# Optimization experiments

Measured on AMD Instinct MI355X. Metric: run time of the kernel, lower is better.

Reference implementation:

```python
import jax, jax.numpy as jnp
import numpy as np

C = 256
NUM_HEADS = 4
GROUPS = 32  # max(1, 256//8), divides 256
EPS = 1e-5


def setup_inputs() -> dict:
    key = jax.random.key(0)
    ks = jax.random.split(key, 7)
    B, H, W = 4, 64, 64
    s = 0.02
    return {
        "x": jax.random.normal(ks[0], (B, C, H, W), dtype=jnp.float32),
        "norm_gamma": jnp.ones((C,), jnp.float32),
        "norm_beta": jnp.zeros((C,), jnp.float32),
        "qkv_w": jax.random.normal(ks[1], (3 * C, C), jnp.float32) * s,  # 1x1 conv kernel squeezed
        "qkv_b": jax.random.normal(ks[2], (3 * C,), jnp.float32) * s,
        "proj_w": jax.random.normal(ks[3], (C, C), jnp.float32) * s,
        "proj_b": jax.random.normal(ks[4], (C,), jnp.float32) * s,
    }


def reference(x, norm_gamma, norm_beta, qkv_w, qkv_b, proj_w, proj_b):
    B, Cc, H, W = x.shape
    hd = Cc // NUM_HEADS
    scale = hd ** -0.5

    # GroupNorm over (channels-per-group, H, W)
    xg = x.reshape(B, GROUPS, Cc // GROUPS, H, W)
    mu = xg.mean(axis=(2, 3, 4), keepdims=True)
    var = xg.var(axis=(2, 3, 4), keepdims=True)
    h = ((xg - mu) * jax.lax.rsqrt(var + EPS)).reshape(B, Cc, H, W)
    h = h * norm_gamma[:, None, None] + norm_beta[:, None, None]

    # 1x1 conv QKV: [B,3C,H,W]
    qkv = jnp.einsum('bchw,oc->bohw', h, qkv_w) + qkv_b[:, None, None]
    q, k, v = jnp.split(qkv, 3, axis=1)

    def heads(t):  # [B,C,H,W] -> [B,nh,HW,hd]
        return t.reshape(B, NUM_HEADS, hd, H * W).transpose(0, 1, 3, 2)

    q, k, v = heads(q), heads(k), heads(v)
    attn = jnp.einsum('bhnd,bhmd->bhnm', q, k) * scale  # [B,nh,HW,HW]
    attn = jax.nn.softmax(attn, axis=-1)
    out = jnp.einsum('bhnm,bhmd->bhnd', attn, v)  # [B,nh,HW,hd]
    out = out.transpose(0, 1, 3, 2).reshape(B, Cc, H, W)

    out = jnp.einsum('bchw,oc->bohw', out, proj_w) + proj_b[:, None, None]
    return x + out
```

## Files before the change

### kernel.cpp

```cpp
#include <hip/hip_runtime.h>
#include <hip/hip_bf16.h>
#include <stdint.h>

typedef unsigned short u16;
typedef __attribute__((ext_vector_type(8))) short bf16x8;
typedef __attribute__((ext_vector_type(4))) float f32x4;
typedef __attribute__((ext_vector_type(16))) float f32x16;

#define HW 4096
#define CC 256
#define QSCALE 0.18033688011112042f

__device__ __forceinline__ u16 f2bf(float f) {
    union { float f; uint32_t i; } v; v.f = f;
    uint32_t x = v.i;
    return (u16)((x + 0x7fffu + ((x >> 16) & 1u)) >> 16);
}

__device__ __forceinline__ float fast_exp2(float x) {
#if __has_builtin(__builtin_amdgcn_exp2f)
    return __builtin_amdgcn_exp2f(x);
#else
    return exp2f(x);
#endif
}

__device__ __forceinline__ unsigned cvt_pk_bf16(float lo, float hi) {
    unsigned r;
    asm("v_cvt_pk_bf16_f32 %0, %1, %2" : "=v"(r) : "v"(lo), "v"(hi));
    return r;
}

__device__ __forceinline__ void plane_swap(unsigned& a, unsigned& b) {
#if __has_builtin(__builtin_amdgcn_permlane32_swap)
    auto r = __builtin_amdgcn_permlane32_swap(a, b, false, false);
    a = r[0]; b = r[1];
#else
    unsigned ax = __shfl_xor((int)a, 32);
    unsigned bx = __shfl_xor((int)b, 32);
    bool hi = (threadIdx.x & 32) != 0;
    unsigned na = hi ? bx : a;
    unsigned nb = hi ? b : ax;
    a = na; b = nb;
#endif
}

#define MFMA16(a, b, c) __builtin_amdgcn_mfma_f32_16x16x32_bf16(a, b, c, 0, 0, 0)
#define MFMA32(a, b, c) __builtin_amdgcn_mfma_f32_32x32x16_bf16(a, b, c, 0, 0, 0)

__global__ void k_wsc(const float* __restrict__ qkv_w, const float* __restrict__ proj_w,
                      const float* __restrict__ x,
                      u16* __restrict__ wqkv, u16* __restrict__ wproj, float* __restrict__ stats) {
    int bid = blockIdx.x;
    if (bid < 128) {
        int bg = bid;
        const float4* p = reinterpret_cast<const float4*>(x + (size_t)bg * 8 * HW);
        float s = 0.f, ss = 0.f;
        for (int i = 0; i < 32; ++i) {
            float4 v = p[threadIdx.x + i * 256];
            s += v.x + v.y + v.z + v.w;
            ss += v.x * v.x + v.y * v.y + v.z * v.z + v.w * v.w;
        }
        __shared__ float rs[256], rss[256];
        rs[threadIdx.x] = s; rss[threadIdx.x] = ss;
        __syncthreads();
        for (int off = 128; off > 0; off >>= 1) {
            if (threadIdx.x < off) { rs[threadIdx.x] += rs[threadIdx.x + off]; rss[threadIdx.x] += rss[threadIdx.x + off]; }
            __syncthreads();
        }
        if (threadIdx.x == 0) {
            float mu = rs[0] * (1.f / 32768.f);
            float var = rss[0] * (1.f / 32768.f) - mu * mu;
            stats[bg * 2] = mu;
            stats[bg * 2 + 1] = rsqrtf(var + 1e-5f);
        }
    } else {
        int i = (bid - 128) * 256 + threadIdx.x;
        if (i < 768 * 256) {
            int o = i >> 8;
            float sc = (o < 256) ? QSCALE : 1.0f;
            wqkv[i] = f2bf(qkv_w[i] * sc);
        }
        int j = i - 768 * 256;
        if (j >= 0 && j < 256 * 256) wproj[j] = f2bf(proj_w[j]);
    }
}

__global__ __launch_bounds__(256) void k_gnt(const float* __restrict__ x, const float* __restrict__ stats,
                                             const float* __restrict__ gamma, const float* __restrict__ beta,
                                             u16* __restrict__ h_t) {
    int bid = blockIdx.x;
    int b = bid >> 8;
    int cb = (bid >> 6) & 3;
    int nb = bid & 63;
    int t = threadIdx.x;
    int cl = t >> 2;
    int ch = t & 3;
    int c = cb * 64 + cl;
    int g = c >> 3;
    float mu = stats[(b * 32 + g) * 2];
    float rsg = stats[(b * 32 + g) * 2 + 1];
    float ga = gamma[c], be = beta[c];
    __shared__ float T[64][66];
    const float4* p = reinterpret_cast<const float4*>(x + ((size_t)(b * CC + c)) * HW + nb * 64 + ch * 16);
    for (int j = 0; j < 4; ++j) {
        float4 v = p[j];
        int nbase = ch * 16 + j * 4;
        T[nbase + 0][cl] = (v.x - mu) * rsg * ga + be;
        T[nbase + 1][cl] = (v.y - mu) * rsg * ga + be;
        T[nbase + 2][cl] = (v.z - mu) * rsg * ga + be;
        T[nbase + 3][cl] = (v.w - mu) * rsg * ga + be;
    }
    __syncthreads();
    int nl = t >> 2;
    union { u16 u[16]; uint4 q[2]; } pk;
    for (int j = 0; j < 16; ++j) pk.u[j] = f2bf(T[nl][ch * 16 + j]);
    u16* dst = h_t + ((size_t)b * HW + nb * 64 + nl) * CC + cb * 64 + ch * 16;
    *reinterpret_cast<uint4*>(dst) = pk.q[0];
    *reinterpret_cast<uint4*>(dst + 8) = pk.q[1];
}

__global__ __launch_bounds__(256) void k_qkv(const u16* __restrict__ wqkv, const u16* __restrict__ h_t,
                                             const float* __restrict__ qkv_b,
                                             u16* __restrict__ qk_t, u16* __restrict__ v_o) {
    int bid = blockIdx.x;
    int b = bid / 192;
    int rem = bid % 192;
    int om = rem >> 5;
    int nb = rem & 31;
    int o0 = om * 128, n0 = nb * 128;
    int t = threadIdx.x;
    int wid = t >> 6, lane = t & 63;
    int wm = wid >> 1, wn = wid & 1;
    int l15 = lane & 15, lg = lane >> 4;

    __shared__ u16 sA[128 * 40], sB[128 * 40];
    f32x4 acc[4][4];
    for (int i = 0; i < 4; ++i) for (int j = 0; j < 4; ++j) acc[i][j] = (f32x4)0.f;

    const u16* gA = wqkv + (size_t)o0 * 256;
    const u16* gB = h_t + ((size_t)b * HW + n0) * CC;
    int row = t >> 1, half = t & 1;

    for (int kt = 0; kt < 8; ++kt) {
        __syncthreads();
        {
            const uint4* pa = reinterpret_cast<const uint4*>(gA + (size_t)row * 256 + kt * 32 + half * 16);
            uint4 a0 = pa[0], a1 = pa[1];
            const uint4* pb = reinterpret_cast<const uint4*>(gB + (size_t)row * 256 + kt * 32 + half * 16);
            uint4 b0 = pb[0], b1 = pb[1];
            *reinterpret_cast<uint4*>(&sA[row * 40 + half * 16]) = a0;
            *reinterpret_cast<uint4*>(&sA[row * 40 + half * 16 + 8]) = a1;
            *reinterpret_cast<uint4*>(&sB[row * 40 + half * 16]) = b0;
            *reinterpret_cast<uint4*>(&sB[row * 40 + half * 16 + 8]) = b1;
        }
        __syncthreads();
        bf16x8 af[4], bfr[4];
        for (int mt = 0; mt < 4; ++mt)
            af[mt] = *reinterpret_cast<const bf16x8*>(&sA[(wm * 64 + mt * 16 + l15) * 40 + lg * 8]);
        for (int nt = 0; nt < 4; ++nt)
            bfr[nt] = *reinterpret_cast<const bf16x8*>(&sB[(wn * 64 + nt * 16 + l15) * 40 + lg * 8]);
        for (int mt = 0; mt < 4; ++mt)
            for (int nt = 0; nt < 4; ++nt)
                acc[mt][nt] = MFMA16(af[mt], bfr[nt], acc[mt][nt]);
    }

    if (o0 < 512) {
        for (int mt = 0; mt < 4; ++mt) {
            int ob = o0 + wm * 64 + mt * 16 + lg * 4;
            float bias[4];
            for (int r = 0; r < 4; ++r) {
                int o = ob + r;
                bias[r] = qkv_b[o] * (o < 256 ? QSCALE : 1.0f);
            }
            for (int nt = 0; nt < 4; ++nt) {
                int n = n0 + wn * 64 + nt * 16 + l15;
                union { u16 u[4]; uint2 q; } pk;
                for (int r = 0; r < 4; ++r) pk.u[r] = f2bf(acc[mt][nt][r] + bias[r]);
                *reinterpret_cast<uint2*>(qk_t + ((size_t)b * HW + n) * 512 + ob) = pk.q;
            }
        }
    } else {
        for (int mt = 0; mt < 4; ++mt) {
            int ob = o0 + wm * 64 + mt * 16 + lg * 4;
            for (int nt = 0; nt < 4; ++nt) {
                int n = n0 + wn * 64 + nt * 16 + l15;
                for (int r = 0; r < 4; ++r) {
                    int o = ob + r;
                    float bias = qkv_b[o];
                    v_o[((size_t)b * 256 + (o - 512)) * HW + n] = f2bf(acc[mt][nt][r] + bias);
                }
            }
        }
    }
}

__global__ __launch_bounds__(256, 4) void k_attn(const u16* __restrict__ qk_t, const u16* __restrict__ v_o,
                                                 u16* __restrict__ ao_t) {
    int bid = blockIdx.x;
    int swz = (bid & 7) * 64 + (bid >> 3);
    int qb = swz & 31, head = (swz >> 5) & 3, b = swz >> 7;
    int n0 = qb * 128;
    int t = threadIdx.x;
    int wq = t >> 6;
    int lane = t & 63, l31 = lane & 31, h = lane >> 5;

    __shared__ u16 lds[2 * 2 * 64 * 72];

    const u16* qbase = qk_t + ((size_t)b * HW + n0 + wq * 32 + l31) * 512 + head * 64 + h * 8;
    bf16x8 qf[4];
#pragma unroll
    for (int cs = 0; cs < 4; ++cs) qf[cs] = *reinterpret_cast<const bf16x8*>(qbase + cs * 16);

    const u16* gK = qk_t + (size_t)b * HW * 512 + 256 + head * 64;
    const u16* gV = v_o + ((size_t)b * 256 + head * 64) * (size_t)HW;

    int sop = t >> 7;
    int tIn = t & 127;
    int srow = tIn >> 1, shalf = tIn & 1;
    const u16* pS;
    long step;
    if (sop == 0) { pS = gK + (size_t)srow * 512 + shalf * 32; step = 64 * 512; }
    else          { pS = gV + (size_t)srow * HW + shalf * 32;  step = 64; }
    uint4 a0 = *reinterpret_cast<const uint4*>(pS);
    uint4 a1 = *reinterpret_cast<const uint4*>(pS + 8);
    uint4 a2 = *reinterpret_cast<const uint4*>(pS + 16);
    uint4 a3 = *reinterpret_cast<const uint4*>(pS + 24);

    f32x16 o0 = (f32x16)0.f, o1 = (f32x16)0.f;
    float l_run = 0.f;

    for (int ti = 0; ti < 64; ++ti) {
        int buf = ti & 1;
        u16* w = lds + buf * 9216 + sop * 4608 + srow * 72 + shalf * 32;
        *reinterpret_cast<uint4*>(w) = a0;
        *reinterpret_cast<uint4*>(w + 8) = a1;
        *reinterpret_cast<uint4*>(w + 16) = a2;
        *reinterpret_cast<uint4*>(w + 24) = a3;
        if (ti < 63) {
            pS += step;
            a0 = *reinterpret_cast<const uint4*>(pS);
            a1 = *reinterpret_cast<const uint4*>(pS + 8);
            a2 = *reinterpret_cast<const uint4*>(pS + 16);
            a3 = *reinterpret_cast<const uint4*>(pS + 24);
        }
        __syncthreads();

        const u16* bK = lds + buf * 9216;
        const u16* bV = bK + 4608;

        f32x16 s0 = (f32x16)0.f, s1 = (f32x16)0.f;
#pragma unroll
        for (int cs = 0; cs < 4; ++cs) {
            bf16x8 k0 = *reinterpret_cast<const bf16x8*>(bK + l31 * 72 + cs * 16 + h * 8);
            bf16x8 k1 = *reinterpret_cast<const bf16x8*>(bK + (l31 + 32) * 72 + cs * 16 + h * 8);
            s0 = MFMA32(k0, qf[cs], s0);
            s1 = MFMA32(k1, qf[cs], s1);
        }

        float ps = 0.f;
#pragma unroll
        for (int i = 0; i < 16; ++i) { float e = fast_exp2(s0[i]); s0[i] = e; ps += e; }
#pragma unroll
        for (int i = 0; i < 16; ++i) { float e = fast_exp2(s1[i]); s1[i] = e; ps += e; }
        l_run += ps;

        unsigned dws[2][8];
#pragma unroll
        for (int a = 0; a < 4; ++a) {
            dws[0][2 * a]     = cvt_pk_bf16(s0[4 * a],     s0[4 * a + 1]);
            dws[0][2 * a + 1] = cvt_pk_bf16(s0[4 * a + 2], s0[4 * a + 3]);
            dws[1][2 * a]     = cvt_pk_bf16(s1[4 * a],     s1[4 * a + 1]);
            dws[1][2 * a + 1] = cvt_pk_bf16(s1[4 * a + 2], s1[4 * a + 3]);
        }
        bf16x8 pf[4];
#pragma unroll
        for (int ks = 0; ks < 4; ++ks) {
            int kt = ks >> 1, sf = ks & 1;
            unsigned A0 = dws[kt][4 * sf + 0], B0 = dws[kt][4 * sf + 2];
            unsigned A1 = dws[kt][4 * sf + 1], B1 = dws[kt][4 * sf + 3];
            plane_swap(A0, B0);
            plane_swap(A1, B1);
            union { unsigned d[4]; bf16x8 v; } u;
            u.d[0] = A0; u.d[1] = A1; u.d[2] = B0; u.d[3] = B1;
            pf[ks] = u.v;
        }

#pragma unroll
        for (int ks = 0; ks < 4; ++ks) {
            bf16x8 v0 = *reinterpret_cast<const bf16x8*>(bV + l31 * 72 + ks * 16 + h * 8);
            bf16x8 v1 = *reinterpret_cast<const bf16x8*>(bV + (l31 + 32) * 72 + ks * 16 + h * 8);
            o0 = MFMA32(v0, pf[ks], o0);
            o1 = MFMA32(v1, pf[ks], o1);
        }
    }

    l_run += __shfl_xor(l_run, 32);
    float inv = 1.0f / l_run;

    u16* E = lds;
    int qrow = wq * 32 + l31;
#pragma unroll
    for (int r = 0; r < 16; ++r) {
        int d = (r & 3) + 8 * (r >> 2) + 4 * h;
        E[qrow * 72 + d]      = f2bf(o0[r] * inv);
        E[qrow * 72 + 32 + d] = f2bf(o1[r] * inv);
    }
    __syncthreads();
#pragma unroll
    for (int i = 0; i < 4; ++i) {
        int item = i * 256 + t;
        int row = item >> 3, cb = item & 7;
        uint4 w = *reinterpret_cast<const uint4*>(E + row * 72 + cb * 8);
        *reinterpret_cast<uint4*>(ao_t + ((size_t)b * HW + n0 + row) * 256 + head * 64 + cb * 8) = w;
    }
}

__global__ __launch_bounds__(256) void k_proj(const u16* __restrict__ wproj, const u16* __restrict__ ao_t,
                                              const float* __restrict__ proj_b, const float* __restrict__ x,
                                              float* __restrict__ out) {
    int bid = blockIdx.x;
    int b = bid >> 6;
    int om = (bid >> 5) & 1;
    int nb = bid & 31;
    int o0 = om * 128, n0 = nb * 128;
    int t = threadIdx.x;
    int wid = t >> 6, lane = t & 63;
    int wm = wid >> 1, wn = wid & 1;
    int l15 = lane & 15, lg = lane >> 4;

    __shared__ u16 sA[128 * 40], sB[128 * 40];
    f32x4 acc[4][4];
    for (int i = 0; i < 4; ++i) for (int j = 0; j < 4; ++j) acc[i][j] = (f32x4)0.f;

    const u16* gA = wproj + (size_t)o0 * 256;
    const u16* gB = ao_t + ((size_t)b * HW + n0) * CC;
    int row = t >> 1, half = t & 1;

    for (int kt = 0; kt < 8; ++kt) {
        __syncthreads();
        {
            const uint4* pa = reinterpret_cast<const uint4*>(gA + (size_t)row * 256 + kt * 32 + half * 16);
            uint4 a0 = pa[0], a1 = pa[1];
            const uint4* pb = reinterpret_cast<const uint4*>(gB + (size_t)row * 256 + kt * 32 + half * 16);
            uint4 b0 = pb[0], b1 = pb[1];
            *reinterpret_cast<uint4*>(&sA[row * 40 + half * 16]) = a0;
            *reinterpret_cast<uint4*>(&sA[row * 40 + half * 16 + 8]) = a1;
            *reinterpret_cast<uint4*>(&sB[row * 40 + half * 16]) = b0;
            *reinterpret_cast<uint4*>(&sB[row * 40 + half * 16 + 8]) = b1;
        }
        __syncthreads();
        bf16x8 af[4], bfr[4];
        for (int mt = 0; mt < 4; ++mt)
            af[mt] = *reinterpret_cast<const bf16x8*>(&sA[(wm * 64 + mt * 16 + l15) * 40 + lg * 8]);
        for (int nt = 0; nt < 4; ++nt)
            bfr[nt] = *reinterpret_cast<const bf16x8*>(&sB[(wn * 64 + nt * 16 + l15) * 40 + lg * 8]);
        for (int mt = 0; mt < 4; ++mt)
            for (int nt = 0; nt < 4; ++nt)
                acc[mt][nt] = MFMA16(af[mt], bfr[nt], acc[mt][nt]);
    }

    for (int mt = 0; mt < 4; ++mt) {
        int ob = o0 + wm * 64 + mt * 16 + lg * 4;
        for (int nt = 0; nt < 4; ++nt) {
            int n = n0 + wn * 64 + nt * 16 + l15;
            for (int r = 0; r < 4; ++r) {
                int o = ob + r;
                size_t idx = ((size_t)(b * CC + o)) * HW + n;
                out[idx] = acc[mt][nt][r] + proj_b[o] + x[idx];
            }
        }
    }
}

extern "C" void kernel_launch(void* const* d_in, const int* in_sizes, int n_in,
                              void* d_out, int out_size, void* d_ws, size_t ws_size,
                              hipStream_t stream) {
    const float* x      = (const float*)d_in[0];
    const float* gamma  = (const float*)d_in[1];
    const float* beta   = (const float*)d_in[2];
    const float* qkv_w  = (const float*)d_in[3];
    const float* qkv_b  = (const float*)d_in[4];
    const float* proj_w = (const float*)d_in[5];
    const float* proj_b = (const float*)d_in[6];
    float* out = (float*)d_out;
    char* ws = (char*)d_ws;

    float* stats = (float*)ws;
    u16* wqkv  = (u16*)(ws + 4096);
    u16* wproj = (u16*)(ws + 4096 + 393216);
    u16* h_t   = (u16*)(ws + 1048576);
    u16* qk_t  = (u16*)(ws + 1048576 + 8388608);
    u16* v_o   = (u16*)(ws + 1048576 + 8388608 + 16777216);
    u16* ao_t  = (u16*)(ws + 1048576 + 8388608 + 16777216 + 8388608);

    k_wsc<<<dim3(1152), dim3(256), 0, stream>>>(qkv_w, proj_w, x, wqkv, wproj, stats);
    k_gnt<<<dim3(1024), dim3(256), 0, stream>>>(x, stats, gamma, beta, h_t);
    k_qkv<<<dim3(768), dim3(256), 0, stream>>>(wqkv, h_t, qkv_b, qk_t, v_o);
    k_attn<<<dim3(512), dim3(256), 0, stream>>>(qk_t, v_o, ao_t);
    k_proj<<<dim3(256), dim3(256), 0, stream>>>(wproj, ao_t, proj_b, x, out);
}
```

Before: 132.4 us.

## Split attention key range across two blocks and add a combine kernel

The attention kernel now splits each query tile's 4096 keys into two halves handled by separate blocks, doubling the grid from 512 to 1024 blocks so more of the GPU is occupied. Each block writes unnormalized fp32 partial outputs and row sums to workspace. A new k_comb kernel adds the two halves, normalizes, and writes the bf16 attention output. The cost is an extra kernel launch and roughly 33 MB of fp32 partial traffic written and read back. The combine relies on the existing softmax using no per-split running max, so the partial sums can be added directly.

```diff
diff --git a/kernel.cpp b/kernel.cpp
--- a/kernel.cpp
+++ b/kernel.cpp
@@ -196,10 +196,11 @@
 }
 
 __global__ __launch_bounds__(256, 4) void k_attn(const u16* __restrict__ qk_t, const u16* __restrict__ v_o,
-                                                 u16* __restrict__ ao_t) {
+                                                 float* __restrict__ op, float* __restrict__ lp) {
     int bid = blockIdx.x;
-    int swz = (bid & 7) * 64 + (bid >> 3);
-    int qb = swz & 31, head = (swz >> 5) & 3, b = swz >> 7;
+    int swz = (bid & 7) * 128 + (bid >> 3);
+    int tile = swz >> 1, kg = swz & 1;
+    int qb = tile & 31, head = (tile >> 5) & 3, b = tile >> 7;
     int n0 = qb * 128;
     int t = threadIdx.x;
     int wq = t >> 6;
@@ -220,8 +221,8 @@
     int srow = tIn >> 1, shalf = tIn & 1;
     const u16* pS;
     long step;
-    if (sop == 0) { pS = gK + (size_t)srow * 512 + shalf * 32; step = 64 * 512; }
-    else          { pS = gV + (size_t)srow * HW + shalf * 32;  step = 64; }
+    if (sop == 0) { pS = gK + (size_t)(kg * 2048 + srow) * 512 + shalf * 32; step = 64 * 512; }
+    else          { pS = gV + (size_t)srow * HW + kg * 2048 + shalf * 32;    step = 64; }
     uint4 a0 = *reinterpret_cast<const uint4*>(pS);
     uint4 a1 = *reinterpret_cast<const uint4*>(pS + 8);
     uint4 a2 = *reinterpret_cast<const uint4*>(pS + 16);
@@ -230,14 +231,14 @@
     f32x16 o0 = (f32x16)0.f, o1 = (f32x16)0.f;
     float l_run = 0.f;
 
-    for (int ti = 0; ti < 64; ++ti) {
+    for (int ti = 0; ti < 32; ++ti) {
         int buf = ti & 1;
         u16* w = lds + buf * 9216 + sop * 4608 + srow * 72 + shalf * 32;
         *reinterpret_cast<uint4*>(w) = a0;
         *reinterpret_cast<uint4*>(w + 8) = a1;
         *reinterpret_cast<uint4*>(w + 16) = a2;
         *reinterpret_cast<uint4*>(w + 24) = a3;
-        if (ti < 63) {
+        if (ti < 31) {
             pS += step;
             a0 = *reinterpret_cast<const uint4*>(pS);
             a1 = *reinterpret_cast<const uint4*>(pS + 8);
@@ -296,15 +297,39 @@
     }
 
     l_run += __shfl_xor(l_run, 32);
-    float inv = 1.0f / l_run;
-
-    u16* E = lds;
+
+    float* P = op + ((((size_t)tile * 2 + kg) * 4 + wq) * 32) * 64 + lane;
+#pragma unroll
+    for (int r = 0; r < 16; ++r) {
+        P[r * 64]        = o0[r];
+        P[(16 + r) * 64] = o1[r];
+    }
+    if (h == 0) lp[(((size_t)tile * 2 + kg) * 4 + wq) * 32 + l31] = l_run;
+}
+
+__global__ __launch_bounds__(256) void k_comb(const float* __restrict__ op, const float* __restrict__ lp,
+                                              u16* __restrict__ ao_t) {
+    int tile = blockIdx.x;
+    int qb = tile & 31, head = (tile >> 5) & 3, b = tile >> 7;
+    int n0 = qb * 128;
+    int t = threadIdx.x;
+    int wq = t >> 6, lane = t & 63, l31 = lane & 31, h = lane >> 5;
+
+    __shared__ u16 E[128 * 72];
+
+    const float* p0 = op + ((((size_t)tile * 2 + 0) * 4 + wq) * 32) * 64 + lane;
+    const float* p1 = op + ((((size_t)tile * 2 + 1) * 4 + wq) * 32) * 64 + lane;
+    float l = lp[(((size_t)tile * 2 + 0) * 4 + wq) * 32 + l31]
+            + lp[(((size_t)tile * 2 + 1) * 4 + wq) * 32 + l31];
+    float inv = 1.0f / l;
     int qrow = wq * 32 + l31;
 #pragma unroll
     for (int r = 0; r < 16; ++r) {
         int d = (r & 3) + 8 * (r >> 2) + 4 * h;
-        E[qrow * 72 + d]      = f2bf(o0[r] * inv);
-        E[qrow * 72 + 32 + d] = f2bf(o1[r] * inv);
+        float a = p0[r * 64] + p1[r * 64];
+        float c = p0[(16 + r) * 64] + p1[(16 + r) * 64];
+        E[qrow * 72 + d]      = f2bf(a * inv);
+        E[qrow * 72 + 32 + d] = f2bf(c * inv);
     }
     __syncthreads();
 #pragma unroll
@@ -390,13 +415,16 @@
     u16* wqkv  = (u16*)(ws + 4096);
     u16* wproj = (u16*)(ws + 4096 + 393216);
     u16* h_t   = (u16*)(ws + 1048576);
-    u16* qk_t  = (u16*)(ws + 1048576 + 8388608);
-    u16* v_o   = (u16*)(ws + 1048576 + 8388608 + 16777216);
-    u16* ao_t  = (u16*)(ws + 1048576 + 8388608 + 16777216 + 8388608);
+    u16* qk_t  = (u16*)(ws + 9437184);
+    u16* v_o   = (u16*)(ws + 26214400);
+    u16* ao_t  = (u16*)(ws + 34603008);
+    float* op  = (float*)(ws + 42991616);
+    float* lp  = (float*)(ws + 76546048);
 
     k_wsc<<<dim3(1152), dim3(256), 0, stream>>>(qkv_w, proj_w, x, wqkv, wproj, stats);
     k_gnt<<<dim3(1024), dim3(256), 0, stream>>>(x, stats, gamma, beta, h_t);
     k_qkv<<<dim3(768), dim3(256), 0, stream>>>(wqkv, h_t, qkv_b, qk_t, v_o);
-    k_attn<<<dim3(512), dim3(256), 0, stream>>>(qk_t, v_o, ao_t);
+    k_attn<<<dim3(1024), dim3(256), 0, stream>>>(qk_t, v_o, op, lp);
+    k_comb<<<dim3(512), dim3(256), 0, stream>>>(op, lp, ao_t);
     k_proj<<<dim3(256), dim3(256), 0, stream>>>(wproj, ao_t, proj_b, x, out);
 }
```

New measurement: 142.1 us. +7.4%, slower.
